# Performance work log

Hardware: AMD Instinct MI355X
Metric: run time of the kernel (lower is better)

The kernel has to match this reference:

```python
import jax, jax.numpy as jnp
import numpy as np

B, T, D = 8, 2048, 512


def setup_inputs() -> dict:
    key = jax.random.key(0)
    k1, _ = jax.random.split(key)
    h = jax.random.normal(k1, (B, T, D), dtype=jnp.float32)
    k = jnp.ones((), dtype=jnp.float32)  # scalar learned decay param, init='ones'
    return {"h": h, "k": k}


def reference(h, k):
    # h: [B, T, D], k: scalar
    Tn = h.shape[1]
    h_cum = jnp.cumsum(h, axis=1)                                   # [B,T,D]
    h_prev = jnp.pad(h[:, :-1, :], ((0, 0), (1, 0), (0, 0)))        # shift right by 1
    delta = h_cum - h_prev
    delta_mag = jnp.linalg.norm(delta, axis=-1)                      # [B,T]
    t = jnp.arange(Tn)[:, None]
    j = jnp.arange(Tn)[None, :]
    dist = jnp.abs(t - j).astype(jnp.float32)
    decay = jnp.exp(-jax.nn.softplus(k) * dist) * (j <= t)           # [T,T] causal decay
    # importance_{b,i,j} = delta_mag_{b,i} * decay_{i,j}; factor delta_mag out of einsum
    context = jnp.einsum('ij,bjd->bid', decay, h)                    # [B,T,D]
    return jnp.abs(delta_mag[..., None] * context)
```

## Files before the change

### kernel.cpp

```cpp
#include <hip/hip_runtime.h>
#include <math.h>

#define BB 8
#define TT 2048
#define DD 512
#define LL 8
#define CC (TT / LL)
#define D4 (DD / 4)
#define NBLK (BB * CC)

__device__ __forceinline__ float get_s(const float* kp) {
    float k = *kp;
    return (k > 20.0f) ? k : log1pf(expf(k));
}

__global__ __launch_bounds__(D4) void k1_chunk(
    const float* __restrict__ h, const float* __restrict__ kp,
    float* __restrict__ csum, float* __restrict__ cend)
{
    const int blk = blockIdx.x;
    const int b = blk / CC, c = blk % CC;
    const int tid = threadIdx.x;
    const float a = expf(-get_s(kp));

    const float4* hp = reinterpret_cast<const float4*>(h)
                     + (size_t)(b * TT + c * LL) * D4 + tid;

    float4 x[LL];
    #pragma unroll
    for (int i = 0; i < LL; i++) x[i] = hp[(size_t)i * D4];

    float sx = 0.f, sy = 0.f, sz = 0.f, sw = 0.f;
    float ex = 0.f, ey = 0.f, ez = 0.f, ew = 0.f;
    #pragma unroll
    for (int i = 0; i < LL; i++) {
        sx += x[i].x; sy += x[i].y; sz += x[i].z; sw += x[i].w;
        ex = fmaf(a, ex, x[i].x);
        ey = fmaf(a, ey, x[i].y);
        ez = fmaf(a, ez, x[i].z);
        ew = fmaf(a, ew, x[i].w);
    }
    const size_t w = (size_t)blk * D4 + tid;
    reinterpret_cast<float4*>(csum)[w] = make_float4(sx, sy, sz, sw);
    reinterpret_cast<float4*>(cend)[w] = make_float4(ex, ey, ez, ew);
}

__global__ __launch_bounds__(128) void k2_scan(
    float* __restrict__ csum, float* __restrict__ cend,
    const float* __restrict__ kp)
{
    const int g = blockIdx.x * 128 + threadIdx.x;
    const int b = g >> 9;
    const int d = g & (DD - 1);
    const float s  = get_s(kp);
    const float aL = expf(-s * (float)LL);

    const size_t base = (size_t)b * CC * DD + d;
    float co = 0.f, cc = 0.f;
    #pragma unroll 16
    for (int c = 0; c < CC; c++) {
        const size_t idx = base + (size_t)c * DD;
        float sv = csum[idx];
        float ev = cend[idx];
        csum[idx] = co;
        cend[idx] = cc;
        co += sv;
        cc = fmaf(aL, cc, ev);
    }
}

__global__ __launch_bounds__(D4) void k3_out(
    const float* __restrict__ h, const float* __restrict__ kp,
    const float* __restrict__ coff, const float* __restrict__ ccar,
    float* __restrict__ out)
{
    const int blk = blockIdx.x;
    const int b = blk / CC, c = blk % CC;
    const int tid = threadIdx.x;
    const int wave = tid >> 6, lane = tid & 63;
    const float a = expf(-get_s(kp));

    const int t0 = c * LL;
    const float4* hp = reinterpret_cast<const float4*>(h)
                     + (size_t)(b * TT + t0) * D4 + tid;

    const size_t ci = (size_t)blk * D4 + tid;
    float4 co4 = reinterpret_cast<const float4*>(coff)[ci];
    float4 cc4 = reinterpret_cast<const float4*>(ccar)[ci];

    float px = 0.f, py = 0.f, pz = 0.f, pw = 0.f;
    if (t0 > 0) {
        float4 pv = hp[-(size_t)D4];
        px = pv.x; py = pv.y; pz = pv.z; pw = pv.w;
    }

    float4 x[LL];
    #pragma unroll
    for (int i = 0; i < LL; i++) x[i] = hp[(size_t)i * D4];

    float r[LL];
    float cox = co4.x, coy = co4.y, coz = co4.z, cow = co4.w;
    #pragma unroll
    for (int i = 0; i < LL; i++) {
        cox += x[i].x; coy += x[i].y; coz += x[i].z; cow += x[i].w;
        float dx = cox - px, dy = coy - py, dz = coz - pz, dw = cow - pw;
        r[i] = dx * dx + dy * dy + dz * dz + dw * dw;
        px = x[i].x; py = x[i].y; pz = x[i].z; pw = x[i].w;
    }

    #pragma unroll
    for (int m = 1; m < 64; m <<= 1) {
        #pragma unroll
        for (int i = 0; i < LL; i++) r[i] += __shfl_xor(r[i], m, 64);
    }

    __shared__ float part[2][LL];
    if (lane == 0) {
        #pragma unroll
        for (int i = 0; i < LL; i++) part[wave][i] = r[i];
    }
    __syncthreads();

    float mag[LL];
    #pragma unroll
    for (int i = 0; i < LL; i++) mag[i] = sqrtf(part[0][i] + part[1][i]);

    float4* op = reinterpret_cast<float4*>(out)
               + (size_t)(b * TT + t0) * D4 + tid;
    float ccx = cc4.x, ccy = cc4.y, ccz = cc4.z, ccw = cc4.w;
    #pragma unroll
    for (int i = 0; i < LL; i++) {
        ccx = fmaf(a, ccx, x[i].x);
        ccy = fmaf(a, ccy, x[i].y);
        ccz = fmaf(a, ccz, x[i].z);
        ccw = fmaf(a, ccw, x[i].w);
        float m = mag[i];
        op[(size_t)i * D4] = make_float4(fabsf(m * ccx), fabsf(m * ccy),
                                         fabsf(m * ccz), fabsf(m * ccw));
    }
}

extern "C" void kernel_launch(void* const* d_in, const int* in_sizes, int n_in,
                              void* d_out, int out_size, void* d_ws, size_t ws_size,
                              hipStream_t stream) {
    const float* h  = (const float*)d_in[0];
    const float* kp = (const float*)d_in[1];
    float* out = (float*)d_out;

    const size_t NS = (size_t)BB * CC * DD;
    float* csum = (float*)d_ws;
    float* cend = csum + NS;

    k1_chunk<<<dim3(NBLK), dim3(D4), 0, stream>>>(h, kp, csum, cend);
    k2_scan <<<dim3(BB * DD / 128), dim3(128), 0, stream>>>(csum, cend, kp);
    k3_out  <<<dim3(NBLK), dim3(D4), 0, stream>>>(h, kp, csum, cend, out);
}
```

Baseline: 110.1 us.

## Parallelize chunk scan across segments and double chunk length

The chunk-carry scan is split into four segments per column. Each segment reduces its partial sum and decayed carry, the segments combine through shared memory, and each then rescans locally. This adds parallelism to a previously serial 256-step scan that ran on only 32 blocks. Chunk length doubles to 16, which halves the scan length and the workspace traffic. The per-thread register arrays of h are replaced by reloading h in the output kernel, trading some extra (likely cached) global reads for lower register pressure.

```diff
diff --git a/kernel.cpp b/kernel.cpp
--- a/kernel.cpp
+++ b/kernel.cpp
@@ -4,10 +4,13 @@
 #define BB 8
 #define TT 2048
 #define DD 512
-#define LL 8
+#define LL 16
 #define CC (TT / LL)
 #define D4 (DD / 4)
 #define NBLK (BB * CC)
+#define SEGS 4
+#define SEGLEN (CC / SEGS)
+#define NCOL (BB * DD)
 
 __device__ __forceinline__ float get_s(const float* kp) {
     float k = *kp;
@@ -26,39 +29,62 @@
     const float4* hp = reinterpret_cast<const float4*>(h)
                      + (size_t)(b * TT + c * LL) * D4 + tid;
 
-    float4 x[LL];
-    #pragma unroll
-    for (int i = 0; i < LL; i++) x[i] = hp[(size_t)i * D4];
-
     float sx = 0.f, sy = 0.f, sz = 0.f, sw = 0.f;
     float ex = 0.f, ey = 0.f, ez = 0.f, ew = 0.f;
     #pragma unroll
     for (int i = 0; i < LL; i++) {
-        sx += x[i].x; sy += x[i].y; sz += x[i].z; sw += x[i].w;
-        ex = fmaf(a, ex, x[i].x);
-        ey = fmaf(a, ey, x[i].y);
-        ez = fmaf(a, ez, x[i].z);
-        ew = fmaf(a, ew, x[i].w);
+        float4 x = hp[(size_t)i * D4];
+        sx += x.x; sy += x.y; sz += x.z; sw += x.w;
+        ex = fmaf(a, ex, x.x);
+        ey = fmaf(a, ey, x.y);
+        ez = fmaf(a, ez, x.z);
+        ew = fmaf(a, ew, x.w);
     }
     const size_t w = (size_t)blk * D4 + tid;
     reinterpret_cast<float4*>(csum)[w] = make_float4(sx, sy, sz, sw);
     reinterpret_cast<float4*>(cend)[w] = make_float4(ex, ey, ez, ew);
 }
 
-__global__ __launch_bounds__(128) void k2_scan(
+__global__ __launch_bounds__(256) void k2_scan(
     float* __restrict__ csum, float* __restrict__ cend,
     const float* __restrict__ kp)
 {
-    const int g = blockIdx.x * 128 + threadIdx.x;
-    const int b = g >> 9;
-    const int d = g & (DD - 1);
-    const float s  = get_s(kp);
-    const float aL = expf(-s * (float)LL);
+    const int tid = threadIdx.x;
+    const int cl  = tid & 63;
+    const int seg = tid >> 6;
+    const int col = blockIdx.x * 64 + cl;
+    const int b = col >> 9;
+    const int d = col & (DD - 1);
+    const float s    = get_s(kp);
+    const float aL   = expf(-s * (float)LL);
+    const float aL32 = expf(-s * (float)(LL * SEGLEN));
 
     const size_t base = (size_t)b * CC * DD + d;
-    float co = 0.f, cc = 0.f;
-    #pragma unroll 16
-    for (int c = 0; c < CC; c++) {
+    const int c0 = seg * SEGLEN;
+
+    float Sa = 0.f, Ea = 0.f;
+    #pragma unroll 8
+    for (int c = c0; c < c0 + SEGLEN; c++) {
+        const size_t idx = base + (size_t)c * DD;
+        Sa += csum[idx];
+        Ea = fmaf(aL, Ea, cend[idx]);
+    }
+
+    __shared__ float sS[SEGS][64];
+    __shared__ float sE[SEGS][64];
+    sS[seg][cl] = Sa;
+    sE[seg][cl] = Ea;
+    __syncthreads();
+
+    float off = 0.f, car = 0.f;
+    for (int sp = 0; sp < seg; sp++) {
+        off += sS[sp][cl];
+        car = fmaf(aL32, car, sE[sp][cl]);
+    }
+
+    float co = off, cc = car;
+    #pragma unroll 8
+    for (int c = c0; c < c0 + SEGLEN; c++) {
         const size_t idx = base + (size_t)c * DD;
         float sv = csum[idx];
         float ev = cend[idx];
@@ -94,18 +120,15 @@
         px = pv.x; py = pv.y; pz = pv.z; pw = pv.w;
     }
 
-    float4 x[LL];
-    #pragma unroll
-    for (int i = 0; i < LL; i++) x[i] = hp[(size_t)i * D4];
-
     float r[LL];
     float cox = co4.x, coy = co4.y, coz = co4.z, cow = co4.w;
     #pragma unroll
     for (int i = 0; i < LL; i++) {
-        cox += x[i].x; coy += x[i].y; coz += x[i].z; cow += x[i].w;
+        float4 x = hp[(size_t)i * D4];
+        cox += x.x; coy += x.y; coz += x.z; cow += x.w;
         float dx = cox - px, dy = coy - py, dz = coz - pz, dw = cow - pw;
         r[i] = dx * dx + dy * dy + dz * dz + dw * dw;
-        px = x[i].x; py = x[i].y; pz = x[i].z; pw = x[i].w;
+        px = x.x; py = x.y; pz = x.z; pw = x.w;
     }
 
     #pragma unroll
@@ -130,10 +153,11 @@
     float ccx = cc4.x, ccy = cc4.y, ccz = cc4.z, ccw = cc4.w;
     #pragma unroll
     for (int i = 0; i < LL; i++) {
-        ccx = fmaf(a, ccx, x[i].x);
-        ccy = fmaf(a, ccy, x[i].y);
-        ccz = fmaf(a, ccz, x[i].z);
-        ccw = fmaf(a, ccw, x[i].w);
+        float4 x = hp[(size_t)i * D4];
+        ccx = fmaf(a, ccx, x.x);
+        ccy = fmaf(a, ccy, x.y);
+        ccz = fmaf(a, ccz, x.z);
+        ccw = fmaf(a, ccw, x.w);
         float m = mag[i];
         op[(size_t)i * D4] = make_float4(fabsf(m * ccx), fabsf(m * ccy),
                                          fabsf(m * ccz), fabsf(m * ccw));
@@ -152,6 +176,6 @@
     float* cend = csum + NS;
 
     k1_chunk<<<dim3(NBLK), dim3(D4), 0, stream>>>(h, kp, csum, cend);
-    k2_scan <<<dim3(BB * DD / 128), dim3(128), 0, stream>>>(csum, cend, kp);
+    k2_scan <<<dim3(NCOL * SEGS / 256), dim3(256), 0, stream>>>(csum, cend, kp);
     k3_out  <<<dim3(NBLK), dim3(D4), 0, stream>>>(h, kp, csum, cend, out);
 }
```

Result: faster. 99.70 us (-9.4%).
